# Optimization experiments

Hardware: AMD Instinct MI355X
Metric: run time of the kernel (lower is better)

## Reference

```python
import jax, jax.numpy as jnp
import numpy as np

NODE_FEAT_DIM = 140
CONFIG_FEAT_DIM = 24
N_OPS = 120
OP_EMB_DIM = 8
H_DIM = 64
N_LAYERS = 3
N_NODES = 5000
N_EDGES = 8000
N_CONFIGS = 32
IN_DIM = NODE_FEAT_DIM + OP_EMB_DIM + CONFIG_FEAT_DIM  # 172


def setup_inputs() -> dict:
    key = jax.random.key(0)
    ks = jax.random.split(key, 24)
    s = 0.05
    inp = {
        'node_feat': jax.random.normal(ks[0], (1, N_NODES, NODE_FEAT_DIM), jnp.float32),
        'node_opcode': jax.random.randint(ks[1], (1, N_NODES), 0, N_OPS, jnp.int64),
        'edge_index': jax.random.randint(ks[2], (1, N_EDGES, 2), 0, N_NODES, jnp.int64),
        'config_feat': jax.random.normal(ks[3], (1, N_CONFIGS, CONFIG_FEAT_DIM), jnp.float32),
        'op_emb': jax.random.normal(ks[4], (N_OPS, OP_EMB_DIM), jnp.float32) * s,
        # layer 0 SAGE weights (in_dim=172), layers 1..2 stacked (h->h)
        'w_self0': jax.random.normal(ks[5], (IN_DIM, H_DIM), jnp.float32) * s,
        'w_neigh0': jax.random.normal(ks[6], (IN_DIM, H_DIM), jnp.float32) * s,
        'b0': jnp.zeros((H_DIM,), jnp.float32),
        'w_self': jax.random.normal(ks[7], (N_LAYERS - 1, H_DIM, H_DIM), jnp.float32) * s,
        'w_neigh': jax.random.normal(ks[8], (N_LAYERS - 1, H_DIM, H_DIM), jnp.float32) * s,
        'b': jnp.zeros((N_LAYERS - 1, H_DIM), jnp.float32),
        'skip_w': jax.random.normal(ks[9], (N_LAYERS, H_DIM, H_DIM), jnp.float32) * s,
        'skip_b': jnp.zeros((N_LAYERS, H_DIM), jnp.float32),
        'p1_w': jax.random.normal(ks[10], (N_LAYERS * H_DIM, (N_LAYERS - 1) * H_DIM), jnp.float32) * s,
        'p1_b': jnp.zeros(((N_LAYERS - 1) * H_DIM,), jnp.float32),
        'p2_w': jax.random.normal(ks[11], ((N_LAYERS - 1) * H_DIM, H_DIM), jnp.float32) * s,
        'p2_b': jnp.zeros((H_DIM,), jnp.float32),
        'p3_w': jax.random.normal(ks[12], (H_DIM, 1), jnp.float32) * s,
        'p3_b': jnp.zeros((1,), jnp.float32),
    }
    return inp


def _sage(x, src, dst, w_self, w_neigh, bias):
    # x: (N, C, D); bidirectional mean aggregation over edges, then linear + ReLU
    n = x.shape[0]
    msg = jax.ops.segment_sum(x[src], dst, num_segments=n)          # (N, C, D)
    deg = jax.ops.segment_sum(jnp.ones(src.shape, x.dtype), dst, num_segments=n)
    agg = msg / jnp.maximum(deg, 1.0)[:, None, None]
    return jax.nn.relu(jnp.einsum('ncd,dh->nch', x, w_self)
                       + jnp.einsum('ncd,dh->nch', agg, w_neigh) + bias)


def reference(node_feat, node_opcode, edge_index, config_feat,
              op_emb, w_self0, w_neigh0, b0, w_self, w_neigh, b,
              skip_w, skip_b, p1_w, p1_b, p2_w, p2_b, p3_w, p3_b):
    nf = node_feat[0]                     # (N, 140)
    op = node_opcode[0]                   # (N,)
    ei = edge_index[0]                    # (M, 2)
    cf = config_feat[0]                   # (C, 24)
    n_nodes, n_configs = nf.shape[0], cf.shape[0]

    # early join: node feats + op embedding broadcast with config feats
    xn = jnp.concatenate([nf, op_emb[op]], axis=-1)                     # (N, 148)
    x = jnp.concatenate([
        jnp.broadcast_to(xn[:, None, :], (n_nodes, n_configs, xn.shape[-1])),
        jnp.broadcast_to(cf[None, :, :], (n_nodes, n_configs, cf.shape[-1])),
    ], axis=-1)                                                          # (N, C, 172)

    # bidirectional edge list
    src = jnp.concatenate([ei[:, 0], ei[:, 1]])
    dst = jnp.concatenate([ei[:, 1], ei[:, 0]])

    skips = []
    x = _sage(x, src, dst, w_self0, w_neigh0, b0)
    skips.append(jax.nn.relu(jnp.einsum('nch,hk->nck', x, skip_w[0]) + skip_b[0]))
    for l in range(N_LAYERS - 1):
        x = _sage(x, src, dst, w_self[l], w_neigh[l], b[l])
        skips.append(jax.nn.relu(jnp.einsum('nch,hk->nck', x, skip_w[l + 1]) + skip_b[l + 1]))

    x = jnp.concatenate(skips, axis=-1)          # (N, C, 3*H)
    x = x.sum(axis=0)                            # global_add_pool over nodes -> (C, 3*H)
    x = jax.nn.relu(x @ p1_w + p1_b)
    x = jax.nn.relu(x @ p2_w + p2_b)
    return (x @ p3_w + p3_b)[:, 0]               # (C,)
```

## Files before the change

### kernel.cpp

```cpp
#include <hip/hip_runtime.h>

#define N_NODESC 5000
#define N_EDGESC 8000
#define NCFG 32
#define HDIM 64
#define NF_DIM 140
#define OPE_DIM 8
#define XN_DIM 148
#define CF_DIM 24
#define NBLK 1250

using f32x4 = __attribute__((ext_vector_type(4))) float;
using bf16x8 = __attribute__((ext_vector_type(8))) short;

__device__ __forceinline__ ushort f2b(float f) {
    uint u = __float_as_uint(f);
    u += 0x7FFF + ((u >> 16) & 1);
    return (ushort)(u >> 16);
}
__device__ __forceinline__ float b2f(ushort u) {
    return __uint_as_float(((uint)u) << 16);
}

__global__ void k_deg(const int* __restrict__ ei, int* __restrict__ deg) {
    int t = blockIdx.x * blockDim.x + threadIdx.x;
    if (t >= 2 * N_EDGESC) return;
    int d;
    if (t < N_EDGESC) d = ei[2 * t + 1];
    else d = ei[2 * (t - N_EDGESC)];
    atomicAdd(&deg[d], 1);
}

__global__ void k_scan(const int* __restrict__ deg, int* __restrict__ row_ptr) {
    __shared__ int ssum[1024];
    int t = threadIdx.x;
    const int per = (N_NODESC + 1023) / 1024;
    int vals[8];
    int loc = 0;
    for (int i = 0; i < per; ++i) {
        int idx = t * per + i;
        int v = (idx < N_NODESC) ? deg[idx] : 0;
        vals[i] = loc;
        loc += v;
    }
    ssum[t] = loc;
    __syncthreads();
    for (int s = 1; s < 1024; s <<= 1) {
        int v = (t >= s) ? ssum[t - s] : 0;
        __syncthreads();
        ssum[t] += v;
        __syncthreads();
    }
    int excl = ssum[t] - loc;
    for (int i = 0; i < per; ++i) {
        int idx = t * per + i;
        if (idx < N_NODESC) row_ptr[idx] = excl + vals[i];
    }
    if (t == 1023) row_ptr[N_NODESC] = ssum[1023];
}

__global__ void k_fill(const int* __restrict__ ei, const int* __restrict__ row_ptr,
                       int* __restrict__ fill, int* __restrict__ col) {
    int t = blockIdx.x * blockDim.x + threadIdx.x;
    if (t >= 2 * N_EDGESC) return;
    int s, d;
    if (t < N_EDGESC) { s = ei[2 * t]; d = ei[2 * t + 1]; }
    else { int e = t - N_EDGESC; s = ei[2 * e + 1]; d = ei[2 * e]; }
    int pos = atomicAdd(&fill[d], 1);
    col[row_ptr[d] + pos] = s;
}

__global__ __launch_bounds__(512) void k_pack(const float* __restrict__ skw,
                                              const float* __restrict__ wsl,
                                              const float* __restrict__ wnl,
                                              const float* __restrict__ cf,
                                              const float* __restrict__ Ws0,
                                              const float* __restrict__ Wn0,
                                              const float* __restrict__ b0,
                                              ushort* __restrict__ frag,
                                              float* __restrict__ Fc,
                                              float* __restrict__ Gc) {
    int m = blockIdx.x;
    int t = threadIdx.x;
    if (m == 7) {
        for (int i = t; i < NCFG * HDIM; i += 512) {
            int c = i >> 6, k = i & 63;
            float f = b0[k], g = 0.f;
            for (int d = 0; d < CF_DIM; ++d) {
                float v = cf[c * CF_DIM + d];
                f += v * Ws0[(XN_DIM + d) * HDIM + k];
                g += v * Wn0[(XN_DIM + d) * HDIM + k];
            }
            Fc[i] = f;
            Gc[i] = g;
        }
        return;
    }
    const float* W;
    switch (m) {
        case 0: W = skw; break;
        case 1: W = wsl; break;
        case 2: W = wnl; break;
        case 3: W = skw + 4096; break;
        case 4: W = wsl + 4096; break;
        case 5: W = wnl + 4096; break;
        default: W = skw + 8192; break;
    }
    int ktnt = t >> 6, lane = t & 63;
    int kt = ktnt >> 2, nt = ktnt & 3;
    int g = lane >> 4, row16 = lane & 15;
    bf16x8 v;
#pragma unroll
    for (int j = 0; j < 8; ++j)
        v[j] = (short)f2b(W[(kt * 32 + g * 8 + j) * HDIM + nt * 16 + row16]);
    *reinterpret_cast<bf16x8*>(frag + (size_t)m * 4096 + (size_t)t * 8) = v;
}

__global__ void k_proj(const float* __restrict__ nf, const int* __restrict__ opcode,
                       const float* __restrict__ op_emb,
                       const float* __restrict__ Ws0, const float* __restrict__ Wn0,
                       float* __restrict__ xs, float* __restrict__ yn) {
    int t = blockIdx.x * blockDim.x + threadIdx.x;
    if (t >= N_NODESC * HDIM) return;
    int n = t >> 6, k = t & 63;
    const float* x = nf + (size_t)n * NF_DIM;
    float s = 0.f, y = 0.f;
    for (int d = 0; d < NF_DIM; ++d) {
        float v = x[d];
        s += v * Ws0[d * HDIM + k];
        y += v * Wn0[d * HDIM + k];
    }
    const float* oe = op_emb + (size_t)opcode[n] * OPE_DIM;
    for (int d = 0; d < OPE_DIM; ++d) {
        float v = oe[d];
        s += v * Ws0[(NF_DIM + d) * HDIM + k];
        y += v * Wn0[(NF_DIM + d) * HDIM + k];
    }
    xs[t] = s;
    yn[t] = y;
}

__global__ void k_En2(const float* __restrict__ xs, const float* __restrict__ yn,
                      const int* __restrict__ row_ptr, const int* __restrict__ col,
                      float* __restrict__ En) {
    int t = blockIdx.x * blockDim.x + threadIdx.x;
    if (t >= N_NODESC * HDIM) return;
    int n = t >> 6, k = t & 63;
    int rs = row_ptr[n], re = row_ptr[n + 1];
    float s = 0.f;
    for (int j = rs; j < re; ++j) s += yn[col[j] * HDIM + k];
    float inv = (re > rs) ? 1.f / (float)(re - rs) : 0.f;
    En[t] = xs[t] + s * inv;
}

__global__ __launch_bounds__(256) void k_h0skip(
    const float* __restrict__ En, const float* __restrict__ Fc,
    const float* __restrict__ Gc, const int* __restrict__ row_ptr,
    const ushort* __restrict__ fragSk, const float* __restrict__ skB,
    ushort* __restrict__ h0, float* __restrict__ partials) {
    __shared__ float sred[4][NCFG * HDIM];
    int lane = threadIdx.x & 63;
    int row16 = lane & 15, g = lane >> 4;
    int w = threadIdx.x >> 6;
    int n = (blockIdx.x * 256 + threadIdx.x) >> 6;

    bf16x8 bSk[2][4];
#pragma unroll
    for (int kt = 0; kt < 2; ++kt)
#pragma unroll
        for (int nt = 0; nt < 4; ++nt)
            bSk[kt][nt] = *reinterpret_cast<const bf16x8*>(
                fragSk + ((kt * 4 + nt) * 64 + lane) * 8);
    float sb[4];
#pragma unroll
    for (int nt = 0; nt < 4; ++nt) sb[nt] = skB[nt * 16 + row16];

    float fcv[2][2][8], gcv[2][2][8];
#pragma unroll
    for (int mt = 0; mt < 2; ++mt)
#pragma unroll
        for (int kt = 0; kt < 2; ++kt) {
            int base = (row16 + 16 * mt) * HDIM + kt * 32 + g * 8;
            float4 f0 = *(const float4*)&Fc[base];
            float4 f1 = *(const float4*)&Fc[base + 4];
            float4 g0 = *(const float4*)&Gc[base];
            float4 g1 = *(const float4*)&Gc[base + 4];
            fcv[mt][kt][0] = f0.x; fcv[mt][kt][1] = f0.y; fcv[mt][kt][2] = f0.z; fcv[mt][kt][3] = f0.w;
            fcv[mt][kt][4] = f1.x; fcv[mt][kt][5] = f1.y; fcv[mt][kt][6] = f1.z; fcv[mt][kt][7] = f1.w;
            gcv[mt][kt][0] = g0.x; gcv[mt][kt][1] = g0.y; gcv[mt][kt][2] = g0.z; gcv[mt][kt][3] = g0.w;
            gcv[mt][kt][4] = g1.x; gcv[mt][kt][5] = g1.y; gcv[mt][kt][6] = g1.z; gcv[mt][kt][7] = g1.w;
        }

    float sc = (row_ptr[n + 1] > row_ptr[n]) ? 1.f : 0.f;
    const float* enp = En + (size_t)n * HDIM;
    float en[2][8];
#pragma unroll
    for (int kt = 0; kt < 2; ++kt) {
        float4 e0 = *(const float4*)&enp[kt * 32 + g * 8];
        float4 e1 = *(const float4*)&enp[kt * 32 + g * 8 + 4];
        en[kt][0] = e0.x; en[kt][1] = e0.y; en[kt][2] = e0.z; en[kt][3] = e0.w;
        en[kt][4] = e1.x; en[kt][5] = e1.y; en[kt][6] = e1.z; en[kt][7] = e1.w;
    }
    bf16x8 aH[2][2];
#pragma unroll
    for (int mt = 0; mt < 2; ++mt)
#pragma unroll
        for (int kt = 0; kt < 2; ++kt) {
            bf16x8 a;
#pragma unroll
            for (int j = 0; j < 8; ++j) {
                float hv = fmaxf(en[kt][j] + fcv[mt][kt][j] + sc * gcv[mt][kt][j], 0.f);
                a[j] = (short)f2b(hv);
            }
            aH[mt][kt] = a;
            *reinterpret_cast<bf16x8*>(
                h0 + (size_t)n * (NCFG * HDIM) + (row16 + 16 * mt) * HDIM + kt * 32 + g * 8) = a;
        }
    f32x4 skipAcc[2][4];
#pragma unroll
    for (int mt = 0; mt < 2; ++mt)
#pragma unroll
        for (int nt = 0; nt < 4; ++nt) {
            f32x4 c2 = f32x4{0.f, 0.f, 0.f, 0.f};
#pragma unroll
            for (int kt = 0; kt < 2; ++kt)
                c2 = __builtin_amdgcn_mfma_f32_16x16x32_bf16(aH[mt][kt], bSk[kt][nt], c2, 0, 0, 0);
#pragma unroll
            for (int r = 0; r < 4; ++r)
                skipAcc[mt][nt][r] = fmaxf(c2[r] + sb[nt], 0.f);
        }

#pragma unroll
    for (int mt = 0; mt < 2; ++mt)
#pragma unroll
        for (int nt = 0; nt < 4; ++nt)
#pragma unroll
            for (int r = 0; r < 4; ++r)
                sred[w][(16 * mt + 4 * g + r) * HDIM + 16 * nt + row16] = skipAcc[mt][nt][r];
    __syncthreads();
    float* pb = partials + (size_t)blockIdx.x * (NCFG * HDIM);
#pragma unroll
    for (int q = 0; q < 2; ++q) {
        int p = threadIdx.x * 8 + q * 4;
        f32x4 s = *(const f32x4*)&sred[0][p];
        s += *(const f32x4*)&sred[1][p];
        s += *(const f32x4*)&sred[2][p];
        s += *(const f32x4*)&sred[3][p];
        *(f32x4*)&pb[p] = s;
    }
}

template <int STORE_H>
__global__ __launch_bounds__(256) void k_sage_mfma(
    const ushort* __restrict__ h_in, ushort* __restrict__ h_out,
    const ushort* __restrict__ fragWs, const ushort* __restrict__ fragWn,
    const ushort* __restrict__ fragSk,
    const float* __restrict__ bias, const float* __restrict__ skB,
    const int* __restrict__ row_ptr, const int* __restrict__ col,
    float* __restrict__ partials) {
    __shared__ __align__(16) char smem_raw[NCFG * HDIM * 4 * 4];
    int lane = threadIdx.x & 63;
    int row16 = lane & 15, g = lane >> 4;
    int w = threadIdx.x >> 6;
    int n = (blockIdx.x * 256 + threadIdx.x) >> 6;
    ushort* st = (ushort*)smem_raw + (size_t)w * (32 * 72);
    float* sredw = (float*)smem_raw;

    bf16x8 bWs[2][4], bWn[2][4], bSk[2][4];
#pragma unroll
    for (int kt = 0; kt < 2; ++kt)
#pragma unroll
        for (int nt = 0; nt < 4; ++nt) {
            int fo = ((kt * 4 + nt) * 64 + lane) * 8;
            bWs[kt][nt] = *reinterpret_cast<const bf16x8*>(fragWs + fo);
            bWn[kt][nt] = *reinterpret_cast<const bf16x8*>(fragWn + fo);
            bSk[kt][nt] = *reinterpret_cast<const bf16x8*>(fragSk + fo);
        }
    float bb[4], sb[4];
#pragma unroll
    for (int nt = 0; nt < 4; ++nt) {
        bb[nt] = bias[nt * 16 + row16];
        sb[nt] = skB[nt * 16 + row16];
    }

    int loff[2][2];
#pragma unroll
    for (int mt = 0; mt < 2; ++mt)
#pragma unroll
        for (int kt = 0; kt < 2; ++kt)
            loff[mt][kt] = (row16 + 16 * mt) * HDIM + kt * 32 + g * 8;

    const ushort* hb = h_in + (size_t)n * (NCFG * HDIM);
    bf16x8 aS[2][2];
#pragma unroll
    for (int mt = 0; mt < 2; ++mt)
#pragma unroll
        for (int kt = 0; kt < 2; ++kt)
            aS[mt][kt] = *reinterpret_cast<const bf16x8*>(hb + loff[mt][kt]);

    float agg[2][2][8];
#pragma unroll
    for (int mt = 0; mt < 2; ++mt)
#pragma unroll
        for (int kt = 0; kt < 2; ++kt)
#pragma unroll
            for (int j = 0; j < 8; ++j) agg[mt][kt][j] = 0.f;
    int rs = row_ptr[n], re = row_ptr[n + 1];
    for (int e = rs; e < re; ++e) {
        const ushort* nb = h_in + (size_t)col[e] * (NCFG * HDIM);
#pragma unroll
        for (int mt = 0; mt < 2; ++mt)
#pragma unroll
            for (int kt = 0; kt < 2; ++kt) {
                bf16x8 u = *reinterpret_cast<const bf16x8*>(nb + loff[mt][kt]);
#pragma unroll
                for (int j = 0; j < 8; ++j) agg[mt][kt][j] += b2f((ushort)u[j]);
            }
    }
    float inv = (re > rs) ? 1.f / (float)(re - rs) : 0.f;
    bf16x8 aA[2][2];
#pragma unroll
    for (int mt = 0; mt < 2; ++mt)
#pragma unroll
        for (int kt = 0; kt < 2; ++kt)
#pragma unroll
            for (int j = 0; j < 8; ++j)
                aA[mt][kt][j] = (short)f2b(agg[mt][kt][j] * inv);

    f32x4 C[2][4];
#pragma unroll
    for (int mt = 0; mt < 2; ++mt)
#pragma unroll
        for (int nt = 0; nt < 4; ++nt) {
            f32x4 c = f32x4{0.f, 0.f, 0.f, 0.f};
#pragma unroll
            for (int kt = 0; kt < 2; ++kt) {
                c = __builtin_amdgcn_mfma_f32_16x16x32_bf16(aS[mt][kt], bWs[kt][nt], c, 0, 0, 0);
                c = __builtin_amdgcn_mfma_f32_16x16x32_bf16(aA[mt][kt], bWn[kt][nt], c, 0, 0, 0);
            }
            C[mt][nt] = c;
        }

#pragma unroll
    for (int mt = 0; mt < 2; ++mt)
#pragma unroll
        for (int nt = 0; nt < 4; ++nt)
#pragma unroll
            for (int r = 0; r < 4; ++r) {
                float hv = fmaxf(C[mt][nt][r] + bb[nt], 0.f);
                st[(16 * mt + 4 * g + r) * 72 + 16 * nt + row16] = f2b(hv);
            }
    asm volatile("s_waitcnt lgkmcnt(0)" ::: "memory");

    if (STORE_H) {
#pragma unroll
        for (int i = 0; i < 4; ++i) {
            int e2 = i * 512 + lane * 8;
            int cc = e2 >> 6, dd = e2 & 63;
            bf16x8 v = *reinterpret_cast<const bf16x8*>(st + cc * 72 + dd);
            *reinterpret_cast<bf16x8*>(h_out + (size_t)n * (NCFG * HDIM) + e2) = v;
        }
    }

    bf16x8 aH[2][2];
#pragma unroll
    for (int mt = 0; mt < 2; ++mt)
#pragma unroll
        for (int kt = 0; kt < 2; ++kt)
            aH[mt][kt] = *reinterpret_cast<const bf16x8*>(
                st + (row16 + 16 * mt) * 72 + kt * 32 + g * 8);
    asm volatile("s_waitcnt lgkmcnt(0)" ::: "memory");
    f32x4 skipAcc[2][4];
#pragma unroll
    for (int mt = 0; mt < 2; ++mt)
#pragma unroll
        for (int nt = 0; nt < 4; ++nt) {
            f32x4 c2 = f32x4{0.f, 0.f, 0.f, 0.f};
#pragma unroll
            for (int kt = 0; kt < 2; ++kt)
                c2 = __builtin_amdgcn_mfma_f32_16x16x32_bf16(aH[mt][kt], bSk[kt][nt], c2, 0, 0, 0);
#pragma unroll
            for (int r = 0; r < 4; ++r)
                skipAcc[mt][nt][r] = fmaxf(c2[r] + sb[nt], 0.f);
        }

    __syncthreads();
#pragma unroll
    for (int mt = 0; mt < 2; ++mt)
#pragma unroll
        for (int nt = 0; nt < 4; ++nt)
#pragma unroll
            for (int r = 0; r < 4; ++r)
                sredw[(size_t)w * (NCFG * HDIM) +
                      (16 * mt + 4 * g + r) * HDIM + 16 * nt + row16] = skipAcc[mt][nt][r];
    __syncthreads();
    float* pb = partials + (size_t)blockIdx.x * (NCFG * HDIM);
#pragma unroll
    for (int q = 0; q < 2; ++q) {
        int p = threadIdx.x * 8 + q * 4;
        f32x4 s = *(const f32x4*)&sredw[0 * NCFG * HDIM + p];
        s += *(const f32x4*)&sredw[1 * NCFG * HDIM + p];
        s += *(const f32x4*)&sredw[2 * NCFG * HDIM + p];
        s += *(const f32x4*)&sredw[3 * NCFG * HDIM + p];
        *(f32x4*)&pb[p] = s;
    }
}

__global__ __launch_bounds__(256) void k_redA(const float* __restrict__ pAll,
                                              float* __restrict__ part2) {
    int i = blockIdx.x * 256 + threadIdx.x;
    int jb = blockIdx.y;
    int l = blockIdx.z;
    const int seg = (NBLK + 31) / 32;
    const float* base = pAll + (size_t)l * NBLK * (NCFG * HDIM);
    float s = 0.f;
    for (int q = 0; q < seg; ++q) {
        int b = jb * seg + q;
        if (b < NBLK) s += base[(size_t)b * (NCFG * HDIM) + i];
    }
    part2[((size_t)l * 32 + jb) * (NCFG * HDIM) + i] = s;
}

__global__ void k_mlp(const float* __restrict__ part2,
                      const float* __restrict__ p1w, const float* __restrict__ p1b,
                      const float* __restrict__ p2w, const float* __restrict__ p2b,
                      const float* __restrict__ p3w, const float* __restrict__ p3b,
                      float* __restrict__ out) {
    int c = blockIdx.x;
    int t = threadIdx.x;
    __shared__ float sx[192];
    __shared__ float h1[128];
    __shared__ float h2[64];
    if (t < 192) {
        int l = t >> 6, k = t & 63;
        float s = 0.f;
#pragma unroll
        for (int b = 0; b < 32; ++b)
            s += part2[((size_t)l * 32 + b) * (NCFG * HDIM) + c * HDIM + k];
        sx[t] = s;
    }
    __syncthreads();
    if (t < 128) {
        float s = p1b[t];
        for (int d = 0; d < 192; ++d) s += sx[d] * p1w[d * 128 + t];
        h1[t] = fmaxf(s, 0.f);
    }
    __syncthreads();
    if (t < 64) {
        float s = p2b[t];
        for (int d = 0; d < 128; ++d) s += h1[d] * p2w[d * 64 + t];
        h2[t] = fmaxf(s, 0.f);
    }
    __syncthreads();
    if (t == 0) {
        float s = p3b[0];
        for (int d = 0; d < 64; ++d) s += h2[d] * p3w[d];
        out[c] = s;
    }
}

extern "C" void kernel_launch(void* const* d_in, const int* in_sizes, int n_in,
                              void* d_out, int out_size, void* d_ws, size_t ws_size,
                              hipStream_t stream) {
    const float* nf  = (const float*)d_in[0];
    const int*   opc = (const int*)d_in[1];
    const int*   ei  = (const int*)d_in[2];
    const float* cf  = (const float*)d_in[3];
    const float* ope = (const float*)d_in[4];
    const float* ws0 = (const float*)d_in[5];
    const float* wn0 = (const float*)d_in[6];
    const float* b0  = (const float*)d_in[7];
    const float* wsl = (const float*)d_in[8];
    const float* wnl = (const float*)d_in[9];
    const float* bl  = (const float*)d_in[10];
    const float* skw = (const float*)d_in[11];
    const float* skb = (const float*)d_in[12];
    const float* p1w = (const float*)d_in[13];
    const float* p1b = (const float*)d_in[14];
    const float* p2w = (const float*)d_in[15];
    const float* p2b = (const float*)d_in[16];
    const float* p3w = (const float*)d_in[17];
    const float* p3b = (const float*)d_in[18];
    float* out = (float*)d_out;

    char* w = (char*)d_ws;
    auto alloc = [&](size_t bytes) {
        char* p = w;
        w += (bytes + 255) & ~(size_t)255;
        return p;
    };
    int* deg      = (int*)alloc(N_NODESC * 4);
    int* fill     = (int*)alloc(N_NODESC * 4);
    int* row_ptr  = (int*)alloc((N_NODESC + 1) * 4);
    int* col      = (int*)alloc(2 * N_EDGESC * 4);
    float* xs     = (float*)alloc((size_t)N_NODESC * HDIM * 4);
    float* yn     = (float*)alloc((size_t)N_NODESC * HDIM * 4);
    float* En     = (float*)alloc((size_t)N_NODESC * HDIM * 4);
    float* Fc     = (float*)alloc(NCFG * HDIM * 4);
    float* Gc     = (float*)alloc(NCFG * HDIM * 4);
    float* part2  = (float*)alloc(3 * 32 * NCFG * HDIM * 4);
    ushort* frag  = (ushort*)alloc(7 * 4096 * 2);
    float* pAll   = (float*)alloc((size_t)3 * NBLK * NCFG * HDIM * 4);
    ushort* h0    = (ushort*)alloc((size_t)N_NODESC * NCFG * HDIM * 2);
    ushort* h1    = (ushort*)alloc((size_t)N_NODESC * NCFG * HDIM * 2);

    float* p0 = pAll;
    float* p1 = pAll + (size_t)NBLK * (NCFG * HDIM);
    float* p2 = pAll + (size_t)2 * NBLK * (NCFG * HDIM);

    hipMemsetAsync(deg, 0, ((N_NODESC * 4 + 255) & ~255) * 2, stream);
    k_deg<<<(2 * N_EDGESC + 255) / 256, 256, 0, stream>>>(ei, deg);
    k_scan<<<1, 1024, 0, stream>>>(deg, row_ptr);
    k_fill<<<(2 * N_EDGESC + 255) / 256, 256, 0, stream>>>(ei, row_ptr, fill, col);
    k_pack<<<8, 512, 0, stream>>>(skw, wsl, wnl, cf, ws0, wn0, b0, frag, Fc, Gc);
    k_proj<<<(N_NODESC * HDIM + 255) / 256, 256, 0, stream>>>(nf, opc, ope, ws0, wn0, xs, yn);
    k_En2<<<(N_NODESC * HDIM + 255) / 256, 256, 0, stream>>>(xs, yn, row_ptr, col, En);

    k_h0skip<<<NBLK, 256, 0, stream>>>(En, Fc, Gc, row_ptr, frag, skb, h0, p0);
    k_sage_mfma<1><<<NBLK, 256, 0, stream>>>(
        h0, h1, frag + 1 * 4096, frag + 2 * 4096, frag + 3 * 4096,
        bl, skb + 64, row_ptr, col, p1);
    k_sage_mfma<0><<<NBLK, 256, 0, stream>>>(
        h1, (ushort*)nullptr, frag + 4 * 4096, frag + 5 * 4096, frag + 6 * 4096,
        bl + 64, skb + 2 * 64, row_ptr, col, p2);

    dim3 gA(8, 32, 3);
    k_redA<<<gA, 256, 0, stream>>>(pAll, part2);
    k_mlp<<<NCFG, 256, 0, stream>>>(part2, p1w, p1b, p2w, p2b, p3w, p3b, out);
}
```

Measured before the change: 149.6 us.

## Fuse CSR build into one kernel and fold self-projection/aggregation into h0skip

The memset plus deg, scan and fill kernels are replaced by a single one-block kernel that counts degrees, scans and fills col using shared-memory atomics. The self projection (xs) and the neighbour-mean En computation move into k_h0skip, which removes the xs and En global buffers and two kernel launches. In k_sage_mfma the skip-weight fragment load is deferred to the point where it is used, which lowers live register pressure. The cost is that edge processing now runs serially inside one block, and k_h0skip does extra per-node work before its MFMA phase.

Result: slower. 171.7 us (+14.8%).

```diff
diff --git a/kernel.cpp b/kernel.cpp
--- a/kernel.cpp
+++ b/kernel.cpp
@@ -22,24 +22,25 @@
     return __uint_as_float(((uint)u) << 16);
 }
 
-__global__ void k_deg(const int* __restrict__ ei, int* __restrict__ deg) {
-    int t = blockIdx.x * blockDim.x + threadIdx.x;
-    if (t >= 2 * N_EDGESC) return;
-    int d;
-    if (t < N_EDGESC) d = ei[2 * t + 1];
-    else d = ei[2 * (t - N_EDGESC)];
-    atomicAdd(&deg[d], 1);
-}
-
-__global__ void k_scan(const int* __restrict__ deg, int* __restrict__ row_ptr) {
+__global__ __launch_bounds__(1024) void k_graph(const int* __restrict__ ei,
+                                                int* __restrict__ row_ptr,
+                                                int* __restrict__ col) {
+    __shared__ int sdeg[N_NODESC];
     __shared__ int ssum[1024];
     int t = threadIdx.x;
+    for (int i = t; i < N_NODESC; i += 1024) sdeg[i] = 0;
+    __syncthreads();
+    for (int e = t; e < 2 * N_EDGESC; e += 1024) {
+        int d = (e < N_EDGESC) ? ei[2 * e + 1] : ei[2 * (e - N_EDGESC)];
+        atomicAdd(&sdeg[d], 1);
+    }
+    __syncthreads();
     const int per = (N_NODESC + 1023) / 1024;
     int vals[8];
     int loc = 0;
     for (int i = 0; i < per; ++i) {
         int idx = t * per + i;
-        int v = (idx < N_NODESC) ? deg[idx] : 0;
+        int v = (idx < N_NODESC) ? sdeg[idx] : 0;
         vals[i] = loc;
         loc += v;
     }
@@ -57,17 +58,19 @@
         if (idx < N_NODESC) row_ptr[idx] = excl + vals[i];
     }
     if (t == 1023) row_ptr[N_NODESC] = ssum[1023];
-}
-
-__global__ void k_fill(const int* __restrict__ ei, const int* __restrict__ row_ptr,
-                       int* __restrict__ fill, int* __restrict__ col) {
-    int t = blockIdx.x * blockDim.x + threadIdx.x;
-    if (t >= 2 * N_EDGESC) return;
-    int s, d;
-    if (t < N_EDGESC) { s = ei[2 * t]; d = ei[2 * t + 1]; }
-    else { int e = t - N_EDGESC; s = ei[2 * e + 1]; d = ei[2 * e]; }
-    int pos = atomicAdd(&fill[d], 1);
-    col[row_ptr[d] + pos] = s;
+    __syncthreads();
+    for (int i = 0; i < per; ++i) {
+        int idx = t * per + i;
+        if (idx < N_NODESC) sdeg[idx] = excl + vals[i];
+    }
+    __syncthreads();
+    for (int e = t; e < 2 * N_EDGESC; e += 1024) {
+        int s, d;
+        if (e < N_EDGESC) { s = ei[2 * e]; d = ei[2 * e + 1]; }
+        else { int e2 = e - N_EDGESC; s = ei[2 * e2 + 1]; d = ei[2 * e2]; }
+        int pos = atomicAdd(&sdeg[d], 1);
+        col[pos] = s;
+    }
 }
 
 __global__ __launch_bounds__(512) void k_pack(const float* __restrict__ skw,
@@ -118,52 +121,49 @@
 
 __global__ void k_proj(const float* __restrict__ nf, const int* __restrict__ opcode,
                        const float* __restrict__ op_emb,
-                       const float* __restrict__ Ws0, const float* __restrict__ Wn0,
-                       float* __restrict__ xs, float* __restrict__ yn) {
+                       const float* __restrict__ Wn0, float* __restrict__ yn) {
     int t = blockIdx.x * blockDim.x + threadIdx.x;
     if (t >= N_NODESC * HDIM) return;
     int n = t >> 6, k = t & 63;
     const float* x = nf + (size_t)n * NF_DIM;
-    float s = 0.f, y = 0.f;
-    for (int d = 0; d < NF_DIM; ++d) {
-        float v = x[d];
-        s += v * Ws0[d * HDIM + k];
-        y += v * Wn0[d * HDIM + k];
-    }
+    float y = 0.f;
+    for (int d = 0; d < NF_DIM; ++d) y += x[d] * Wn0[d * HDIM + k];
     const float* oe = op_emb + (size_t)opcode[n] * OPE_DIM;
-    for (int d = 0; d < OPE_DIM; ++d) {
-        float v = oe[d];
-        s += v * Ws0[(NF_DIM + d) * HDIM + k];
-        y += v * Wn0[(NF_DIM + d) * HDIM + k];
-    }
-    xs[t] = s;
+#pragma unroll
+    for (int d = 0; d < OPE_DIM; ++d) y += oe[d] * Wn0[(NF_DIM + d) * HDIM + k];
     yn[t] = y;
 }
 
-__global__ void k_En2(const float* __restrict__ xs, const float* __restrict__ yn,
-                      const int* __restrict__ row_ptr, const int* __restrict__ col,
-                      float* __restrict__ En) {
-    int t = blockIdx.x * blockDim.x + threadIdx.x;
-    if (t >= N_NODESC * HDIM) return;
-    int n = t >> 6, k = t & 63;
-    int rs = row_ptr[n], re = row_ptr[n + 1];
-    float s = 0.f;
-    for (int j = rs; j < re; ++j) s += yn[col[j] * HDIM + k];
-    float inv = (re > rs) ? 1.f / (float)(re - rs) : 0.f;
-    En[t] = xs[t] + s * inv;
-}
-
 __global__ __launch_bounds__(256) void k_h0skip(
-    const float* __restrict__ En, const float* __restrict__ Fc,
-    const float* __restrict__ Gc, const int* __restrict__ row_ptr,
+    const float* __restrict__ nf, const int* __restrict__ opcode,
+    const float* __restrict__ op_emb, const float* __restrict__ Ws0,
+    const float* __restrict__ yn,
+    const float* __restrict__ Fc, const float* __restrict__ Gc,
+    const int* __restrict__ row_ptr, const int* __restrict__ col,
     const ushort* __restrict__ fragSk, const float* __restrict__ skB,
     ushort* __restrict__ h0, float* __restrict__ partials) {
     __shared__ float sred[4][NCFG * HDIM];
+    __shared__ float sen[4][HDIM];
     int lane = threadIdx.x & 63;
     int row16 = lane & 15, g = lane >> 4;
     int w = threadIdx.x >> 6;
     int n = (blockIdx.x * 256 + threadIdx.x) >> 6;
 
+    const float* x = nf + (size_t)n * NF_DIM;
+    float xsv = 0.f;
+    for (int d = 0; d < NF_DIM; ++d) xsv += x[d] * Ws0[d * HDIM + lane];
+    const float* oe = op_emb + (size_t)opcode[n] * OPE_DIM;
+#pragma unroll
+    for (int d = 0; d < OPE_DIM; ++d) xsv += oe[d] * Ws0[(NF_DIM + d) * HDIM + lane];
+
+    int rs = row_ptr[n], re = row_ptr[n + 1];
+    float acc = 0.f;
+    for (int e = rs; e < re; ++e) acc += yn[(size_t)col[e] * HDIM + lane];
+    float inv = (re > rs) ? 1.f / (float)(re - rs) : 0.f;
+    float sc = (re > rs) ? 1.f : 0.f;
+    sen[w][lane] = xsv + acc * inv;
+    asm volatile("s_waitcnt lgkmcnt(0)" ::: "memory");
+
     bf16x8 bSk[2][4];
 #pragma unroll
     for (int kt = 0; kt < 2; ++kt)
@@ -174,6 +174,15 @@
     float sb[4];
 #pragma unroll
     for (int nt = 0; nt < 4; ++nt) sb[nt] = skB[nt * 16 + row16];
+
+    float en[2][8];
+#pragma unroll
+    for (int kt = 0; kt < 2; ++kt) {
+        float4 e0 = *(const float4*)&sen[w][kt * 32 + g * 8];
+        float4 e1 = *(const float4*)&sen[w][kt * 32 + g * 8 + 4];
+        en[kt][0] = e0.x; en[kt][1] = e0.y; en[kt][2] = e0.z; en[kt][3] = e0.w;
+        en[kt][4] = e1.x; en[kt][5] = e1.y; en[kt][6] = e1.z; en[kt][7] = e1.w;
+    }
 
     float fcv[2][2][8], gcv[2][2][8];
 #pragma unroll
@@ -191,16 +200,6 @@
             gcv[mt][kt][4] = g1.x; gcv[mt][kt][5] = g1.y; gcv[mt][kt][6] = g1.z; gcv[mt][kt][7] = g1.w;
         }
 
-    float sc = (row_ptr[n + 1] > row_ptr[n]) ? 1.f : 0.f;
-    const float* enp = En + (size_t)n * HDIM;
-    float en[2][8];
-#pragma unroll
-    for (int kt = 0; kt < 2; ++kt) {
-        float4 e0 = *(const float4*)&enp[kt * 32 + g * 8];
-        float4 e1 = *(const float4*)&enp[kt * 32 + g * 8 + 4];
-        en[kt][0] = e0.x; en[kt][1] = e0.y; en[kt][2] = e0.z; en[kt][3] = e0.w;
-        en[kt][4] = e1.x; en[kt][5] = e1.y; en[kt][6] = e1.z; en[kt][7] = e1.w;
-    }
     bf16x8 aH[2][2];
 #pragma unroll
     for (int mt = 0; mt < 2; ++mt)
@@ -266,7 +265,7 @@
     ushort* st = (ushort*)smem_raw + (size_t)w * (32 * 72);
     float* sredw = (float*)smem_raw;
 
-    bf16x8 bWs[2][4], bWn[2][4], bSk[2][4];
+    bf16x8 bWs[2][4], bWn[2][4];
 #pragma unroll
     for (int kt = 0; kt < 2; ++kt)
 #pragma unroll
@@ -274,7 +273,6 @@
             int fo = ((kt * 4 + nt) * 64 + lane) * 8;
             bWs[kt][nt] = *reinterpret_cast<const bf16x8*>(fragWs + fo);
             bWn[kt][nt] = *reinterpret_cast<const bf16x8*>(fragWn + fo);
-            bSk[kt][nt] = *reinterpret_cast<const bf16x8*>(fragSk + fo);
         }
     float bb[4], sb[4];
 #pragma unroll
@@ -370,6 +368,14 @@
             aH[mt][kt] = *reinterpret_cast<const bf16x8*>(
                 st + (row16 + 16 * mt) * 72 + kt * 32 + g * 8);
     asm volatile("s_waitcnt lgkmcnt(0)" ::: "memory");
+
+    bf16x8 bSk[2][4];
+#pragma unroll
+    for (int kt = 0; kt < 2; ++kt)
+#pragma unroll
+        for (int nt = 0; nt < 4; ++nt)
+            bSk[kt][nt] = *reinterpret_cast<const bf16x8*>(
+                fragSk + ((kt * 4 + nt) * 64 + lane) * 8);
     f32x4 skipAcc[2][4];
 #pragma unroll
     for (int mt = 0; mt < 2; ++mt)
@@ -429,8 +435,8 @@
     int c = blockIdx.x;
     int t = threadIdx.x;
     __shared__ float sx[192];
-    __shared__ float h1[128];
-    __shared__ float h2[64];
+    __shared__ float h1s[128];
+    __shared__ float h2s[64];
     if (t < 192) {
         int l = t >> 6, k = t & 63;
         float s = 0.f;
@@ -443,18 +449,18 @@
     if (t < 128) {
         float s = p1b[t];
         for (int d = 0; d < 192; ++d) s += sx[d] * p1w[d * 128 + t];
-        h1[t] = fmaxf(s, 0.f);
+        h1s[t] = fmaxf(s, 0.f);
     }
     __syncthreads();
     if (t < 64) {
         float s = p2b[t];
-        for (int d = 0; d < 128; ++d) s += h1[d] * p2w[d * 64 + t];
-        h2[t] = fmaxf(s, 0.f);
+        for (int d = 0; d < 128; ++d) s += h1s[d] * p2w[d * 64 + t];
+        h2s[t] = fmaxf(s, 0.f);
     }
     __syncthreads();
     if (t == 0) {
         float s = p3b[0];
-        for (int d = 0; d < 64; ++d) s += h2[d] * p3w[d];
+        for (int d = 0; d < 64; ++d) s += h2s[d] * p3w[d];
         out[c] = s;
     }
 }
@@ -489,13 +495,9 @@
         w += (bytes + 255) & ~(size_t)255;
         return p;
     };
-    int* deg      = (int*)alloc(N_NODESC * 4);
-    int* fill     = (int*)alloc(N_NODESC * 4);
     int* row_ptr  = (int*)alloc((N_NODESC + 1) * 4);
     int* col      = (int*)alloc(2 * N_EDGESC * 4);
-    float* xs     = (float*)alloc((size_t)N_NODESC * HDIM * 4);
     float* yn     = (float*)alloc((size_t)N_NODESC * HDIM * 4);
-    float* En     = (float*)alloc((size_t)N_NODESC * HDIM * 4);
     float* Fc     = (float*)alloc(NCFG * HDIM * 4);
     float* Gc     = (float*)alloc(NCFG * HDIM * 4);
     float* part2  = (float*)alloc(3 * 32 * NCFG * HDIM * 4);
@@ -508,15 +510,12 @@
     float* p1 = pAll + (size_t)NBLK * (NCFG * HDIM);
     float* p2 = pAll + (size_t)2 * NBLK * (NCFG * HDIM);
 
-    hipMemsetAsync(deg, 0, ((N_NODESC * 4 + 255) & ~255) * 2, stream);
-    k_deg<<<(2 * N_EDGESC + 255) / 256, 256, 0, stream>>>(ei, deg);
-    k_scan<<<1, 1024, 0, stream>>>(deg, row_ptr);
-    k_fill<<<(2 * N_EDGESC + 255) / 256, 256, 0, stream>>>(ei, row_ptr, fill, col);
+    k_graph<<<1, 1024, 0, stream>>>(ei, row_ptr, col);
     k_pack<<<8, 512, 0, stream>>>(skw, wsl, wnl, cf, ws0, wn0, b0, frag, Fc, Gc);
-    k_proj<<<(N_NODESC * HDIM + 255) / 256, 256, 0, stream>>>(nf, opc, ope, ws0, wn0, xs, yn);
-    k_En2<<<(N_NODESC * HDIM + 255) / 256, 256, 0, stream>>>(xs, yn, row_ptr, col, En);
-
-    k_h0skip<<<NBLK, 256, 0, stream>>>(En, Fc, Gc, row_ptr, frag, skb, h0, p0);
+    k_proj<<<(N_NODESC * HDIM + 255) / 256, 256, 0, stream>>>(nf, opc, ope, wn0, yn);
+
+    k_h0skip<<<NBLK, 256, 0, stream>>>(nf, opc, ope, ws0, yn, Fc, Gc,
+                                       row_ptr, col, frag, skb, h0, p0);
     k_sage_mfma<1><<<NBLK, 256, 0, stream>>>(
         h0, h1, frag + 1 * 4096, frag + 2 * 4096, frag + 3 * 4096,
         bl, skb + 64, row_ptr, col, p1);
```
